# Kernel optimization log

Measured on AMD Instinct MI355X. Metric: run time of the kernel, lower is better.

## Reference

```python
import jax, jax.numpy as jnp
import numpy as np

N_NODES = 50000
N_EDGES = 800000
IN_CH = 128
OUT_CH = 32
HID = 2 * OUT_CH  # 64


def gcn_layer(x, W, b, src, dst, n):
    """PyG GCNConv: x' = D^-1/2 (A + I) D^-1/2 (x W) + b, flow source->target."""
    h = x @ W  # [n, out]
    # degree on target nodes, +1 for self loop
    deg = jax.ops.segment_sum(jnp.ones(dst.shape[0], h.dtype), dst, num_segments=n) + 1.0
    dis = jax.lax.rsqrt(deg)  # deg^-1/2
    norm = dis[src] * dis[dst]  # [E]
    msg = h[src] * norm[:, None]  # gather + scale, [E, out]
    agg = jax.ops.segment_sum(msg, dst, num_segments=n)  # scatter-add
    # self-loop contribution has norm dis[i]*dis[i] = 1/deg[i]
    return agg + h * (dis * dis)[:, None] + b


def setup_inputs() -> dict:
    key = jax.random.key(0)
    k1, k2, k3, k4, k5, k6 = jax.random.split(key, 6)
    x = jax.random.normal(k1, (N_NODES, IN_CH), dtype=jnp.float32)
    edge_index = jax.random.randint(k2, (2, N_EDGES), 0, N_NODES, dtype=jnp.int64)
    # Glorot-style init for GCN weights
    W1 = jax.random.normal(k3, (IN_CH, HID), dtype=jnp.float32) / np.sqrt(IN_CH)
    b1 = jnp.zeros((HID,), dtype=jnp.float32)
    W2 = jax.random.normal(k4, (HID, OUT_CH), dtype=jnp.float32) / np.sqrt(HID)
    b2 = jnp.zeros((OUT_CH,), dtype=jnp.float32)
    return {"x": x, "W1": W1, "b1": b1, "W2": W2, "b2": b2, "edge_index": edge_index}


def reference(x, W1, b1, W2, b2, edge_index):
    src, dst = edge_index[0], edge_index[1]
    h = jax.nn.relu(gcn_layer(x, W1, b1, src, dst, N_NODES))
    out = gcn_layer(h, W2, b2, src, dst, N_NODES)
    return out
```

## Files before the change

kernel.cpp:

```cpp
#include <hip/hip_runtime.h>
#include <hip/hip_bf16.h>
#include <cstddef>
#include <cstdint>

#define N_NODES 50000
#define N_EDGES 800000
#define IN_CH 128
#define HID 64
#define OUT_CH 32

#define NBUCK 196
#define BCAP2 5120
#define NBLK 256
#define EPB 3125

typedef __attribute__((ext_vector_type(8))) short bf16x8;
typedef __attribute__((ext_vector_type(8))) unsigned short u16x8;
typedef __attribute__((ext_vector_type(4))) float f32x4;

__device__ __forceinline__ unsigned short bf16rne(float f) {
    union { float f; unsigned u; } c; c.f = f;
    unsigned r = c.u + 0x7FFF + ((c.u >> 16) & 1);
    return (unsigned short)(r >> 16);
}
__device__ __forceinline__ float bf16f(unsigned short b) {
    union { unsigned u; float f; } c; c.u = ((unsigned)b) << 16;
    return c.f;
}

__device__ __forceinline__ void load_edge(const void* ei, int flag, int e, int& s, int& d) {
    if (flag) {
        const long long* p = (const long long*)ei;
        s = (int)p[e];
        d = (int)p[e + N_EDGES];
    } else {
        const int* p = (const int*)ei;
        s = p[e];
        d = p[e + N_EDGES];
    }
}

__global__ __launch_bounds__(256) void init_kernel(const unsigned* ei, int* flagp,
                                                   int* __restrict__ cursor) {
    __shared__ unsigned red[256];
    const int t = threadIdx.x;
    unsigned acc = 0;
    for (int i = t; i < 2048; i += 256) acc |= ei[2 * i + 1];
    red[t] = acc;
    __syncthreads();
    for (int off = 128; off > 0; off >>= 1) {
        if (t < off) red[t] |= red[t + off];
        __syncthreads();
    }
    if (t == 0) *flagp = (red[0] == 0) ? 1 : 0;
    if (t < NBUCK) cursor[t] = t * BCAP2;
}

__global__ __launch_bounds__(256) void scatter1_kernel(const void* ei, const int* flagp,
                                                       int* __restrict__ cursor,
                                                       unsigned* __restrict__ packed) {
    __shared__ unsigned cbuf[EPB];
    __shared__ int h[NBUCK];
    __shared__ int lcur[NBUCK];
    const int flag = *flagp;
    const int t = threadIdx.x;
    const int base = blockIdx.x * EPB;
    if (t < NBUCK) h[t] = 0;
    __syncthreads();
    for (int i = t; i < EPB; i += 256) {
        int s, d;
        load_edge(ei, flag, base + i, s, d);
        cbuf[i] = (unsigned)s | ((unsigned)d << 16);
        atomicAdd(&h[d >> 8], 1);
    }
    __syncthreads();
    if (t < NBUCK) lcur[t] = h[t] ? atomicAdd(&cursor[t], h[t]) : 0;
    __syncthreads();
    for (int i = t; i < EPB; i += 256) {
        unsigned p = cbuf[i];
        int b = p >> 24;
        int pos = atomicAdd(&lcur[b], 1);
        packed[pos] = p;
    }
}

__global__ __launch_bounds__(256) void bucket_kernel(const int* __restrict__ cursor,
                                                     unsigned* __restrict__ packed,
                                                     unsigned* __restrict__ rowinfo,
                                                     float* __restrict__ dis) {
    __shared__ int cnt[256];
    __shared__ int pref[256];
    __shared__ int lbuf[BCAP2];
    const int b = blockIdx.x;
    const int nodebase = b << 8;
    const int rbase = b * BCAP2;
    const int bsize = cursor[b] - rbase;
    const int t = threadIdx.x;
    const int nb = min(256, N_NODES - nodebase);

    cnt[t] = 0;
    __syncthreads();
    for (int i = t; i < bsize; i += 256)
        atomicAdd(&cnt[(packed[rbase + i] >> 16) & 255], 1);
    __syncthreads();
    const int deg = cnt[t];
    pref[t] = deg;
    __syncthreads();
    for (int off = 1; off < 256; off <<= 1) {
        int q = (t >= off) ? pref[t - off] : 0;
        __syncthreads();
        pref[t] += q;
        __syncthreads();
    }
    const int excl = pref[t] - deg;
    if (t < nb) {
        rowinfo[nodebase + t] = (unsigned)(rbase + excl) | ((unsigned)deg << 20);
        dis[nodebase + t] = rsqrtf((float)deg + 1.0f);
    }
    __syncthreads();
    cnt[t] = excl;
    __syncthreads();
    for (int i = t; i < bsize; i += 256) {
        unsigned p = packed[rbase + i];
        int pos = atomicAdd(&cnt[(p >> 16) & 255], 1);
        lbuf[pos] = (int)(p & 0xFFFFu);
    }
    __syncthreads();
    for (int i = t; i < bsize; i += 256)
        packed[rbase + i] = (unsigned)lbuf[i];
}

__global__ __launch_bounds__(256) void gemm1_kernel(
        const float* __restrict__ x, const float* __restrict__ W1,
        unsigned short* __restrict__ h1b) {
    __shared__ unsigned short xa[64][136];
    __shared__ unsigned short wb[64][136];
    const int t = threadIdx.x;
    const int w = t >> 6;
    const int l = t & 63;
    const int brow = blockIdx.x * 64;

    for (int f = t; f < 64 * 32; f += 256) {
        int r = f >> 5, c = (f & 31) << 2;
        int gr = brow + r;
        float4 v = (gr < N_NODES) ? *(const float4*)(x + gr * IN_CH + c)
                                  : make_float4(0.f, 0.f, 0.f, 0.f);
        xa[r][c + 0] = bf16rne(v.x); xa[r][c + 1] = bf16rne(v.y);
        xa[r][c + 2] = bf16rne(v.z); xa[r][c + 3] = bf16rne(v.w);
    }
    for (int f = t; f < 128 * 16; f += 256) {
        int k = f >> 4, n = (f & 15) << 2;
        float4 v = *(const float4*)(W1 + k * HID + n);
        wb[n + 0][k] = bf16rne(v.x); wb[n + 1][k] = bf16rne(v.y);
        wb[n + 2][k] = bf16rne(v.z); wb[n + 3][k] = bf16rne(v.w);
    }
    __syncthreads();

    const int fr = l & 15;
    const int fk = (l >> 4) << 3;
    f32x4 acc[4] = {{0.f,0.f,0.f,0.f},{0.f,0.f,0.f,0.f},{0.f,0.f,0.f,0.f},{0.f,0.f,0.f,0.f}};
#pragma unroll
    for (int kb = 0; kb < 4; ++kb) {
        const int k = kb * 32 + fk;
        bf16x8 a = *(const bf16x8*)&xa[w * 16 + fr][k];
#pragma unroll
        for (int n = 0; n < 4; ++n) {
            bf16x8 bfr = *(const bf16x8*)&wb[n * 16 + fr][k];
            acc[n] = __builtin_amdgcn_mfma_f32_16x16x32_bf16(a, bfr, acc[n], 0, 0, 0);
        }
    }
    const int rb = brow + w * 16 + ((l >> 4) << 2);
#pragma unroll
    for (int n = 0; n < 4; ++n) {
#pragma unroll
        for (int i = 0; i < 4; ++i) {
            int r = rb + i;
            if (r < N_NODES) h1b[r * HID + n * 16 + fr] = bf16rne(acc[n][i]);
        }
    }
}

__global__ __launch_bounds__(256) void agg1_kernel(
        const unsigned* __restrict__ rowinfo, const unsigned* __restrict__ sorted,
        const float* __restrict__ dis, const unsigned short* __restrict__ h1b,
        const float* __restrict__ b1, unsigned short* __restrict__ agg1b) {
    const int l = threadIdx.x & 63;
    const int g = l >> 3;
    const int cl = l & 7;
    const int d = blockIdx.x * 4 + (threadIdx.x >> 6);
    if (d >= N_NODES) return;
    const unsigned ri = rowinfo[d];
    const int beg = (int)(ri & 0xFFFFFu);
    const int end = beg + (int)(ri >> 20);
    const float dd = dis[d];
    float a0 = 0.f, a1 = 0.f, a2 = 0.f, a3 = 0.f;
    float a4 = 0.f, a5 = 0.f, a6 = 0.f, a7 = 0.f;
    for (int j = beg + g; j < end; j += 8) {
        int s = (int)sorted[j];
        float n = dis[s] * dd;
        bf16x8 h = *(const bf16x8*)(h1b + s * HID + 8 * cl);
        a0 += bf16f((unsigned short)h[0]) * n; a1 += bf16f((unsigned short)h[1]) * n;
        a2 += bf16f((unsigned short)h[2]) * n; a3 += bf16f((unsigned short)h[3]) * n;
        a4 += bf16f((unsigned short)h[4]) * n; a5 += bf16f((unsigned short)h[5]) * n;
        a6 += bf16f((unsigned short)h[6]) * n; a7 += bf16f((unsigned short)h[7]) * n;
    }
#pragma unroll
    for (int st = 8; st <= 32; st <<= 1) {
        a0 += __shfl_xor(a0, st, 64); a1 += __shfl_xor(a1, st, 64);
        a2 += __shfl_xor(a2, st, 64); a3 += __shfl_xor(a3, st, 64);
        a4 += __shfl_xor(a4, st, 64); a5 += __shfl_xor(a5, st, 64);
        a6 += __shfl_xor(a6, st, 64); a7 += __shfl_xor(a7, st, 64);
    }
    if (g == 0) {
        bf16x8 hs = *(const bf16x8*)(h1b + d * HID + 8 * cl);
        float4 bv0 = *(const float4*)(b1 + 8 * cl);
        float4 bv1 = *(const float4*)(b1 + 8 * cl + 4);
        float d2 = dd * dd;
        u16x8 o;
        o[0] = bf16rne(fmaxf(a0 + bf16f((unsigned short)hs[0]) * d2 + bv0.x, 0.f));
        o[1] = bf16rne(fmaxf(a1 + bf16f((unsigned short)hs[1]) * d2 + bv0.y, 0.f));
        o[2] = bf16rne(fmaxf(a2 + bf16f((unsigned short)hs[2]) * d2 + bv0.z, 0.f));
        o[3] = bf16rne(fmaxf(a3 + bf16f((unsigned short)hs[3]) * d2 + bv0.w, 0.f));
        o[4] = bf16rne(fmaxf(a4 + bf16f((unsigned short)hs[4]) * d2 + bv1.x, 0.f));
        o[5] = bf16rne(fmaxf(a5 + bf16f((unsigned short)hs[5]) * d2 + bv1.y, 0.f));
        o[6] = bf16rne(fmaxf(a6 + bf16f((unsigned short)hs[6]) * d2 + bv1.z, 0.f));
        o[7] = bf16rne(fmaxf(a7 + bf16f((unsigned short)hs[7]) * d2 + bv1.w, 0.f));
        *(u16x8*)(agg1b + d * HID + 8 * cl) = o;
    }
}

__global__ __launch_bounds__(256) void gemm2_kernel(
        const unsigned short* __restrict__ agg1b, const float* __restrict__ W2,
        unsigned short* __restrict__ h2b) {
    __shared__ unsigned short xa[64][72];
    __shared__ unsigned short wb[32][72];
    const int t = threadIdx.x;
    const int w = t >> 6;
    const int l = t & 63;
    const int brow = blockIdx.x * 64;

    for (int f = t; f < 64 * 16; f += 256) {
        int r = f >> 4, c = (f & 15) << 2;
        int gr = brow + r;
        ushort4 v = make_ushort4(0, 0, 0, 0);
        if (gr < N_NODES) v = *(const ushort4*)(agg1b + gr * HID + c);
        *(ushort4*)&xa[r][c] = v;
    }
    for (int f = t; f < 64 * 8; f += 256) {
        int k = f >> 3, n = (f & 7) << 2;
        float4 v = *(const float4*)(W2 + k * OUT_CH + n);
        wb[n + 0][k] = bf16rne(v.x); wb[n + 1][k] = bf16rne(v.y);
        wb[n + 2][k] = bf16rne(v.z); wb[n + 3][k] = bf16rne(v.w);
    }
    __syncthreads();

    const int fr = l & 15;
    const int fk = (l >> 4) << 3;
    f32x4 acc[2] = {{0.f,0.f,0.f,0.f},{0.f,0.f,0.f,0.f}};
#pragma unroll
    for (int kb = 0; kb < 2; ++kb) {
        const int k = kb * 32 + fk;
        bf16x8 a = *(const bf16x8*)&xa[w * 16 + fr][k];
#pragma unroll
        for (int n = 0; n < 2; ++n) {
            bf16x8 bfr = *(const bf16x8*)&wb[n * 16 + fr][k];
            acc[n] = __builtin_amdgcn_mfma_f32_16x16x32_bf16(a, bfr, acc[n], 0, 0, 0);
        }
    }
    const int rb = brow + w * 16 + ((l >> 4) << 2);
#pragma unroll
    for (int n = 0; n < 2; ++n) {
#pragma unroll
        for (int i = 0; i < 4; ++i) {
            int r = rb + i;
            if (r < N_NODES) h2b[r * OUT_CH + n * 16 + fr] = bf16rne(acc[n][i]);
        }
    }
}

__global__ __launch_bounds__(256) void agg2_kernel(
        const unsigned* __restrict__ rowinfo, const unsigned* __restrict__ sorted,
        const float* __restrict__ dis, const unsigned short* __restrict__ h2b,
        const float* __restrict__ b2, float* __restrict__ out) {
    const int l = threadIdx.x & 63;
    const int g = l >> 2;
    const int cl = l & 3;
    const int d = blockIdx.x * 4 + (threadIdx.x >> 6);
    if (d >= N_NODES) return;
    const unsigned ri = rowinfo[d];
    const int beg = (int)(ri & 0xFFFFFu);
    const int end = beg + (int)(ri >> 20);
    const float dd = dis[d];
    float a0 = 0.f, a1 = 0.f, a2 = 0.f, a3 = 0.f;
    float a4 = 0.f, a5 = 0.f, a6 = 0.f, a7 = 0.f;
    for (int j = beg + g; j < end; j += 16) {
        int s = (int)sorted[j];
        float n = dis[s] * dd;
        bf16x8 h = *(const bf16x8*)(h2b + s * OUT_CH + 8 * cl);
        a0 += bf16f((unsigned short)h[0]) * n; a1 += bf16f((unsigned short)h[1]) * n;
        a2 += bf16f((unsigned short)h[2]) * n; a3 += bf16f((unsigned short)h[3]) * n;
        a4 += bf16f((unsigned short)h[4]) * n; a5 += bf16f((unsigned short)h[5]) * n;
        a6 += bf16f((unsigned short)h[6]) * n; a7 += bf16f((unsigned short)h[7]) * n;
    }
#pragma unroll
    for (int st = 4; st <= 32; st <<= 1) {
        a0 += __shfl_xor(a0, st, 64); a1 += __shfl_xor(a1, st, 64);
        a2 += __shfl_xor(a2, st, 64); a3 += __shfl_xor(a3, st, 64);
        a4 += __shfl_xor(a4, st, 64); a5 += __shfl_xor(a5, st, 64);
        a6 += __shfl_xor(a6, st, 64); a7 += __shfl_xor(a7, st, 64);
    }
    if (g == 0) {
        bf16x8 hs = *(const bf16x8*)(h2b + d * OUT_CH + 8 * cl);
        float4 bv0 = *(const float4*)(b2 + 8 * cl);
        float4 bv1 = *(const float4*)(b2 + 8 * cl + 4);
        float d2 = dd * dd;
        float4 o0, o1;
        o0.x = a0 + bf16f((unsigned short)hs[0]) * d2 + bv0.x;
        o0.y = a1 + bf16f((unsigned short)hs[1]) * d2 + bv0.y;
        o0.z = a2 + bf16f((unsigned short)hs[2]) * d2 + bv0.z;
        o0.w = a3 + bf16f((unsigned short)hs[3]) * d2 + bv0.w;
        o1.x = a4 + bf16f((unsigned short)hs[4]) * d2 + bv1.x;
        o1.y = a5 + bf16f((unsigned short)hs[5]) * d2 + bv1.y;
        o1.z = a6 + bf16f((unsigned short)hs[6]) * d2 + bv1.z;
        o1.w = a7 + bf16f((unsigned short)hs[7]) * d2 + bv1.w;
        *(float4*)(out + d * OUT_CH + 8 * cl) = o0;
        *(float4*)(out + d * OUT_CH + 8 * cl + 4) = o1;
    }
}

extern "C" void kernel_launch(void* const* d_in, const int* in_sizes, int n_in,
                              void* d_out, int out_size, void* d_ws, size_t ws_size,
                              hipStream_t stream) {
    const float* x  = (const float*)d_in[0];
    const float* W1 = (const float*)d_in[1];
    const float* b1 = (const float*)d_in[2];
    const float* W2 = (const float*)d_in[3];
    const float* b2 = (const float*)d_in[4];
    const void*  ei = d_in[5];
    float* out = (float*)d_out;

    char* wp = (char*)d_ws;
    auto alloc = [&](size_t n) { char* p = wp; wp += (n + 511) & ~(size_t)511; return p; };
    int*   flagp   = (int*)alloc(4);
    int*   cursor  = (int*)alloc(NBUCK * 4);
    unsigned* rowinfo = (unsigned*)alloc((size_t)N_NODES * 4);
    float* dis     = (float*)alloc((size_t)N_NODES * 4);
    unsigned* packed = (unsigned*)alloc((size_t)NBUCK * BCAP2 * 4);
    unsigned short* h1b = (unsigned short*)alloc((size_t)N_NODES * HID * 2);
    unsigned short* agg1b = (unsigned short*)alloc((size_t)N_NODES * HID * 2);
    unsigned short* h2b = (unsigned short*)alloc((size_t)N_NODES * OUT_CH * 2);

    init_kernel<<<1, 256, 0, stream>>>((const unsigned*)ei, flagp, cursor);
    scatter1_kernel<<<NBLK, 256, 0, stream>>>(ei, flagp, cursor, packed);
    bucket_kernel<<<NBUCK, 256, 0, stream>>>(cursor, packed, rowinfo, dis);

    gemm1_kernel<<<(N_NODES + 63) / 64, 256, 0, stream>>>(x, W1, h1b);

    agg1_kernel<<<(N_NODES + 3) / 4, 256, 0, stream>>>(rowinfo, packed, dis, h1b, b1, agg1b);

    gemm2_kernel<<<(N_NODES + 63) / 64, 256, 0, stream>>>(agg1b, W2, h2b);

    agg2_kernel<<<(N_NODES + 3) / 4, 256, 0, stream>>>(rowinfo, packed, dis, h2b, b2, out);
}
```

Baseline: 94.65 us.

## Fold init into scatter and merge bucket sort with first GEMM launch

The single-block init kernel is removed. Every scatter block now redundantly computes the int64/int32 index-format flag itself, and cursors start at zero via a memset, with the bucket base added on use. The bucket sort and the first GEMM are merged into one launch that branches on block index and shares LDS through a union, so the two independent stages can run concurrently and one launch is saved. In exchange, each scatter block repeats the flag reduction, the merged kernel's LDS footprint is the larger of the two, and the diff leaves an empty dead loop.

```diff
diff --git a/kernel.cpp b/kernel.cpp
--- a/kernel.cpp
+++ b/kernel.cpp
@@ -13,6 +13,7 @@
 #define BCAP2 5120
 #define NBLK 256
 #define EPB 3125
+#define NT1 782
 
 typedef __attribute__((ext_vector_type(8))) short bf16x8;
 typedef __attribute__((ext_vector_type(8))) unsigned short u16x8;
@@ -40,33 +41,39 @@
     }
 }
 
-__global__ __launch_bounds__(256) void init_kernel(const unsigned* ei, int* flagp,
-                                                   int* __restrict__ cursor) {
-    __shared__ unsigned red[256];
-    const int t = threadIdx.x;
-    unsigned acc = 0;
-    for (int i = t; i < 2048; i += 256) acc |= ei[2 * i + 1];
-    red[t] = acc;
-    __syncthreads();
-    for (int off = 128; off > 0; off >>= 1) {
-        if (t < off) red[t] |= red[t + off];
-        __syncthreads();
-    }
-    if (t == 0) *flagp = (red[0] == 0) ? 1 : 0;
-    if (t < NBUCK) cursor[t] = t * BCAP2;
-}
-
-__global__ __launch_bounds__(256) void scatter1_kernel(const void* ei, const int* flagp,
+__global__ __launch_bounds__(256) void scatter1_kernel(const void* ei,
                                                        int* __restrict__ cursor,
                                                        unsigned* __restrict__ packed) {
     __shared__ unsigned cbuf[EPB];
     __shared__ int h[NBUCK];
     __shared__ int lcur[NBUCK];
-    const int flag = *flagp;
+    __shared__ unsigned red[256];
     const int t = threadIdx.x;
     const int base = blockIdx.x * EPB;
+
+    {
+        unsigned acc = 0;
+        const unsigned* w = (const unsigned*)ei;
+        for (int i = t; i < 2048; i += 256) acc |= w[2 * i + 1];
+        red[t] = acc;
+    }
     if (t < NBUCK) h[t] = 0;
     __syncthreads();
+    if (t < 128) red[t] |= red[t + 128];
+    __syncthreads();
+    if (t < 64) red[t] |= red[t + 64];
+    __syncthreads();
+    unsigned o = red[0];
+    for (int i = 1; i < 64; i <<= 1) {  }
+    __syncthreads();
+    if (t == 0) {
+        unsigned q = 0;
+        for (int i = 0; i < 64; ++i) q |= red[i];
+        red[0] = q;
+    }
+    __syncthreads();
+    const int flag = (red[0] == 0) ? 1 : 0;
+
     for (int i = t; i < EPB; i += 256) {
         int s, d;
         load_edge(ei, flag, base + i, s, d);
@@ -74,7 +81,7 @@
         atomicAdd(&h[d >> 8], 1);
     }
     __syncthreads();
-    if (t < NBUCK) lcur[t] = h[t] ? atomicAdd(&cursor[t], h[t]) : 0;
+    if (t < NBUCK) lcur[t] = h[t] ? (t * BCAP2 + atomicAdd(&cursor[t], h[t])) : 0;
     __syncthreads();
     for (int i = t; i < EPB; i += 256) {
         unsigned p = cbuf[i];
@@ -84,98 +91,97 @@
     }
 }
 
-__global__ __launch_bounds__(256) void bucket_kernel(const int* __restrict__ cursor,
-                                                     unsigned* __restrict__ packed,
-                                                     unsigned* __restrict__ rowinfo,
-                                                     float* __restrict__ dis) {
-    __shared__ int cnt[256];
-    __shared__ int pref[256];
-    __shared__ int lbuf[BCAP2];
-    const int b = blockIdx.x;
-    const int nodebase = b << 8;
-    const int rbase = b * BCAP2;
-    const int bsize = cursor[b] - rbase;
-    const int t = threadIdx.x;
-    const int nb = min(256, N_NODES - nodebase);
-
-    cnt[t] = 0;
-    __syncthreads();
-    for (int i = t; i < bsize; i += 256)
-        atomicAdd(&cnt[(packed[rbase + i] >> 16) & 255], 1);
-    __syncthreads();
-    const int deg = cnt[t];
-    pref[t] = deg;
-    __syncthreads();
-    for (int off = 1; off < 256; off <<= 1) {
-        int q = (t >= off) ? pref[t - off] : 0;
-        __syncthreads();
-        pref[t] += q;
-        __syncthreads();
-    }
-    const int excl = pref[t] - deg;
-    if (t < nb) {
-        rowinfo[nodebase + t] = (unsigned)(rbase + excl) | ((unsigned)deg << 20);
-        dis[nodebase + t] = rsqrtf((float)deg + 1.0f);
-    }
-    __syncthreads();
-    cnt[t] = excl;
-    __syncthreads();
-    for (int i = t; i < bsize; i += 256) {
-        unsigned p = packed[rbase + i];
-        int pos = atomicAdd(&cnt[(p >> 16) & 255], 1);
-        lbuf[pos] = (int)(p & 0xFFFFu);
-    }
-    __syncthreads();
-    for (int i = t; i < bsize; i += 256)
-        packed[rbase + i] = (unsigned)lbuf[i];
-}
-
-__global__ __launch_bounds__(256) void gemm1_kernel(
+__global__ __launch_bounds__(256) void buckgemm1_kernel(
+        const int* __restrict__ cursor, unsigned* __restrict__ packed,
+        unsigned* __restrict__ rowinfo, float* __restrict__ dis,
         const float* __restrict__ x, const float* __restrict__ W1,
         unsigned short* __restrict__ h1b) {
-    __shared__ unsigned short xa[64][136];
-    __shared__ unsigned short wb[64][136];
+    __shared__ union {
+        struct { int cnt[256]; int pref[256]; int lbuf[BCAP2]; } bk;
+        struct { unsigned short xa[64][136]; unsigned short wb[64][136]; } g1;
+    } u;
     const int t = threadIdx.x;
-    const int w = t >> 6;
-    const int l = t & 63;
-    const int brow = blockIdx.x * 64;
-
-    for (int f = t; f < 64 * 32; f += 256) {
-        int r = f >> 5, c = (f & 31) << 2;
-        int gr = brow + r;
-        float4 v = (gr < N_NODES) ? *(const float4*)(x + gr * IN_CH + c)
-                                  : make_float4(0.f, 0.f, 0.f, 0.f);
-        xa[r][c + 0] = bf16rne(v.x); xa[r][c + 1] = bf16rne(v.y);
-        xa[r][c + 2] = bf16rne(v.z); xa[r][c + 3] = bf16rne(v.w);
-    }
-    for (int f = t; f < 128 * 16; f += 256) {
-        int k = f >> 4, n = (f & 15) << 2;
-        float4 v = *(const float4*)(W1 + k * HID + n);
-        wb[n + 0][k] = bf16rne(v.x); wb[n + 1][k] = bf16rne(v.y);
-        wb[n + 2][k] = bf16rne(v.z); wb[n + 3][k] = bf16rne(v.w);
-    }
-    __syncthreads();
-
-    const int fr = l & 15;
-    const int fk = (l >> 4) << 3;
-    f32x4 acc[4] = {{0.f,0.f,0.f,0.f},{0.f,0.f,0.f,0.f},{0.f,0.f,0.f,0.f},{0.f,0.f,0.f,0.f}};
-#pragma unroll
-    for (int kb = 0; kb < 4; ++kb) {
-        const int k = kb * 32 + fk;
-        bf16x8 a = *(const bf16x8*)&xa[w * 16 + fr][k];
+
+    if (blockIdx.x < NBUCK) {
+        const int b = blockIdx.x;
+        const int nodebase = b << 8;
+        const int rbase = b * BCAP2;
+        const int bsize = cursor[b];
+        const int nb = min(256, N_NODES - nodebase);
+
+        u.bk.cnt[t] = 0;
+        __syncthreads();
+        for (int i = t; i < bsize; i += 256)
+            atomicAdd(&u.bk.cnt[(packed[rbase + i] >> 16) & 255], 1);
+        __syncthreads();
+        const int deg = u.bk.cnt[t];
+        u.bk.pref[t] = deg;
+        __syncthreads();
+        for (int off = 1; off < 256; off <<= 1) {
+            int q = (t >= off) ? u.bk.pref[t - off] : 0;
+            __syncthreads();
+            u.bk.pref[t] += q;
+            __syncthreads();
+        }
+        const int excl = u.bk.pref[t] - deg;
+        if (t < nb) {
+            rowinfo[nodebase + t] = (unsigned)(rbase + excl) | ((unsigned)deg << 20);
+            dis[nodebase + t] = rsqrtf((float)deg + 1.0f);
+        }
+        __syncthreads();
+        u.bk.cnt[t] = excl;
+        __syncthreads();
+        for (int i = t; i < bsize; i += 256) {
+            unsigned p = packed[rbase + i];
+            int pos = atomicAdd(&u.bk.cnt[(p >> 16) & 255], 1);
+            u.bk.lbuf[pos] = (int)(p & 0xFFFFu);
+        }
+        __syncthreads();
+        for (int i = t; i < bsize; i += 256)
+            packed[rbase + i] = (unsigned)u.bk.lbuf[i];
+    } else {
+        const int w = t >> 6;
+        const int l = t & 63;
+        const int brow = (blockIdx.x - NBUCK) * 64;
+
+        for (int f = t; f < 64 * 32; f += 256) {
+            int r = f >> 5, c = (f & 31) << 2;
+            int gr = brow + r;
+            float4 v = (gr < N_NODES) ? *(const float4*)(x + gr * IN_CH + c)
+                                      : make_float4(0.f, 0.f, 0.f, 0.f);
+            u.g1.xa[r][c + 0] = bf16rne(v.x); u.g1.xa[r][c + 1] = bf16rne(v.y);
+            u.g1.xa[r][c + 2] = bf16rne(v.z); u.g1.xa[r][c + 3] = bf16rne(v.w);
+        }
+        for (int f = t; f < 128 * 16; f += 256) {
+            int k = f >> 4, n = (f & 15) << 2;
+            float4 v = *(const float4*)(W1 + k * HID + n);
+            u.g1.wb[n + 0][k] = bf16rne(v.x); u.g1.wb[n + 1][k] = bf16rne(v.y);
+            u.g1.wb[n + 2][k] = bf16rne(v.z); u.g1.wb[n + 3][k] = bf16rne(v.w);
+        }
+        __syncthreads();
+
+        const int fr = l & 15;
+        const int fk = (l >> 4) << 3;
+        f32x4 acc[4] = {{0.f,0.f,0.f,0.f},{0.f,0.f,0.f,0.f},
+                        {0.f,0.f,0.f,0.f},{0.f,0.f,0.f,0.f}};
+#pragma unroll
+        for (int kb = 0; kb < 4; ++kb) {
+            const int k = kb * 32 + fk;
+            bf16x8 a = *(const bf16x8*)&u.g1.xa[w * 16 + fr][k];
+#pragma unroll
+            for (int n = 0; n < 4; ++n) {
+                bf16x8 bfr = *(const bf16x8*)&u.g1.wb[n * 16 + fr][k];
+                acc[n] = __builtin_amdgcn_mfma_f32_16x16x32_bf16(a, bfr, acc[n], 0, 0, 0);
+            }
+        }
+        const int rb = brow + w * 16 + ((l >> 4) << 2);
 #pragma unroll
         for (int n = 0; n < 4; ++n) {
-            bf16x8 bfr = *(const bf16x8*)&wb[n * 16 + fr][k];
-            acc[n] = __builtin_amdgcn_mfma_f32_16x16x32_bf16(a, bfr, acc[n], 0, 0, 0);
-        }
-    }
-    const int rb = brow + w * 16 + ((l >> 4) << 2);
-#pragma unroll
-    for (int n = 0; n < 4; ++n) {
-#pragma unroll
-        for (int i = 0; i < 4; ++i) {
-            int r = rb + i;
-            if (r < N_NODES) h1b[r * HID + n * 16 + fr] = bf16rne(acc[n][i]);
+#pragma unroll
+            for (int i = 0; i < 4; ++i) {
+                int r = rb + i;
+                if (r < N_NODES) h1b[r * HID + n * 16 + fr] = bf16rne(acc[n][i]);
+            }
         }
     }
 }
@@ -341,7 +347,6 @@
 
     char* wp = (char*)d_ws;
     auto alloc = [&](size_t n) { char* p = wp; wp += (n + 511) & ~(size_t)511; return p; };
-    int*   flagp   = (int*)alloc(4);
     int*   cursor  = (int*)alloc(NBUCK * 4);
     unsigned* rowinfo = (unsigned*)alloc((size_t)N_NODES * 4);
     float* dis     = (float*)alloc((size_t)N_NODES * 4);
@@ -350,15 +355,11 @@
     unsigned short* agg1b = (unsigned short*)alloc((size_t)N_NODES * HID * 2);
     unsigned short* h2b = (unsigned short*)alloc((size_t)N_NODES * OUT_CH * 2);
 
-    init_kernel<<<1, 256, 0, stream>>>((const unsigned*)ei, flagp, cursor);
-    scatter1_kernel<<<NBLK, 256, 0, stream>>>(ei, flagp, cursor, packed);
-    bucket_kernel<<<NBUCK, 256, 0, stream>>>(cursor, packed, rowinfo, dis);
-
-    gemm1_kernel<<<(N_NODES + 63) / 64, 256, 0, stream>>>(x, W1, h1b);
-
+    hipMemsetAsync(cursor, 0, NBUCK * sizeof(int), stream);
+    scatter1_kernel<<<NBLK, 256, 0, stream>>>(ei, cursor, packed);
+    buckgemm1_kernel<<<NBUCK + NT1, 256, 0, stream>>>(cursor, packed, rowinfo, dis,
+                                                      x, W1, h1b);
     agg1_kernel<<<(N_NODES + 3) / 4, 256, 0, stream>>>(rowinfo, packed, dis, h1b, b1, agg1b);
-
     gemm2_kernel<<<(N_NODES + 63) / 64, 256, 0, stream>>>(agg1b, W2, h2b);
-
     agg2_kernel<<<(N_NODES + 3) / 4, 256, 0, stream>>>(rowinfo, packed, dis, h2b, b2, out);
 }
```

Measured after the change: 91.81 us. 1.03x faster.
